# Optimization experiments

Measured on AMD Instinct MI355X. Metric: run time of the kernel, lower is better.

## Reference

```python
import jax, jax.numpy as jnp
import numpy as np

N_U, N_I, D, Q, NNZ, L = 100000, 100000, 64, 128, 3200000, 3
N = N_U + N_I

def setup_inputs() -> dict:
    key = jax.random.key(0)
    ks = jax.random.split(key, 9)
    user_emb = jax.random.normal(ks[0], (N_U, D), dtype=jnp.float32) * 0.1
    item_emb = jax.random.normal(ks[1], (N_I, D), dtype=jnp.float32) * 0.1
    adj_row = jax.random.randint(ks[2], (NNZ,), 0, N, dtype=jnp.int32)
    adj_col = jax.random.randint(ks[3], (NNZ,), 0, N, dtype=jnp.int32)
    # ~degree-normalized values so L-layer propagation stays stable
    adj_vals = jax.random.uniform(ks[4], (NNZ,), dtype=jnp.float32) / 16.0
    ut = jax.random.normal(ks[5], (Q, N_U), dtype=jnp.float32) * (1.0 / np.sqrt(N_U))
    vt = jax.random.normal(ks[6], (Q, N_I), dtype=jnp.float32) * (1.0 / np.sqrt(N_I))
    u_mul_s = jax.random.normal(ks[7], (N_U, Q), dtype=jnp.float32) * 0.1
    v_mul_s = jax.random.normal(ks[8], (N_I, Q), dtype=jnp.float32) * 0.1
    return {"user_emb": user_emb, "item_emb": item_emb, "adj_row": adj_row,
            "adj_col": adj_col, "adj_vals": adj_vals, "ut": ut, "vt": vt,
            "u_mul_s": u_mul_s, "v_mul_s": v_mul_s}

def _spmm(row, col, vals, x):
    # y[r] = sum_{e: row[e]==r} vals[e] * x[col[e]]
    return jax.ops.segment_sum(vals[:, None] * x[col], row, num_segments=N)

def reference(user_emb, item_emb, adj_row, adj_col, adj_vals, ut, vt, u_mul_s, v_mul_s):
    ego = jnp.concatenate([user_emb, item_emb], axis=0)  # [N, D]
    acc = jnp.zeros_like(ego)
    svd_u = jnp.zeros((N_U, D), dtype=ego.dtype)
    svd_i = jnp.zeros((N_I, D), dtype=ego.dtype)
    for _ in range(L):
        ego = _spmm(adj_row, adj_col, adj_vals, ego)
        acc = acc + ego
        ue, ie = ego[:N_U], ego[N_U:]
        ut_eu = ut @ ue            # [Q, D]
        vt_ei = vt @ ie            # [Q, D]
        svd_u = svd_u + u_mul_s @ vt_ei
        svd_i = svd_i + v_mul_s @ ut_eu
    mean = acc / L                 # mean over stacked layer embeddings
    return (mean[:N_U], svd_u, mean[N_U:], svd_i)
```

## Files before the change

kernel.cpp:

```cpp
#include <hip/hip_runtime.h>

constexpr int N_U  = 100000;
constexpr int N_I  = 100000;
constexpr int NTOT = 200000;
constexpr int D    = 64;
constexpr int Q    = 128;
constexpr int NNZ  = 3200000;
constexpr int SEG  = N_U * D;

constexpr int G1_CHUNK = 400;
constexpr int G1_NBLK  = 250;

constexpr int BROWS   = 512;
constexpr int NBUCK   = (NTOT + BROWS - 1) / BROWS;
constexpr int P_CHUNK = 8192;
constexpr int P_NBLK  = (NNZ + P_CHUNK - 1) / P_CHUNK;

constexpr int G2_R    = 64;
constexpr int G2_NBLK = (N_U + G2_R - 1) / G2_R;
constexpr int MSTRIDE = 132;

__device__ __forceinline__ unsigned short f2bf(float f) {
  unsigned int b = __float_as_uint(f);
  return (unsigned short)((b + 0x7fff + ((b >> 16) & 1)) >> 16);
}
__device__ __forceinline__ float bf2f(unsigned short u) {
  return __uint_as_float((unsigned int)u << 16);
}

__global__ void __launch_bounds__(512) k_bhist(const int* __restrict__ row,
                                               int* __restrict__ part) {
  __shared__ int h[NBUCK];
  const int t = threadIdx.x;
  if (t < NBUCK) h[t] = 0;
  __syncthreads();
  const int e0 = blockIdx.x * P_CHUNK;
#pragma unroll
  for (int i = 0; i < P_CHUNK / 512; ++i) {
    int e = e0 + i * 512 + t;
    if (e < NNZ) atomicAdd(&h[row[e] >> 9], 1);
  }
  __syncthreads();
  if (t < NBUCK) part[blockIdx.x * NBUCK + t] = h[t];
}

__global__ void __launch_bounds__(512) k_bscan(int* __restrict__ part,
                                               int* __restrict__ outb,
                                               int* __restrict__ bbase) {
  __shared__ int s[512];
  const int t = threadIdx.x;
  int run = 0;
  if (t < NBUCK) {
    for (int blk = 0; blk < P_NBLK; ++blk) {
      int v = part[blk * NBUCK + t];
      outb[blk * NBUCK + t] = run;
      run += v;
    }
  }
  const int own = (t < NBUCK) ? run : 0;
  s[t] = own;
  __syncthreads();
  for (int off = 1; off < 512; off <<= 1) {
    int y = (t >= off) ? s[t - off] : 0;
    __syncthreads();
    s[t] += y;
    __syncthreads();
  }
  int excl = s[t] - own;
  if (t <= NBUCK) bbase[t] = excl;
}

__global__ void __launch_bounds__(512) k_mscat(const int* __restrict__ row,
                                               const int* __restrict__ col,
                                               const float* __restrict__ val,
                                               const int* __restrict__ outb,
                                               const int* __restrict__ bbase,
                                               int2* __restrict__ ebuck) {
  __shared__ int cur[NBUCK];
  const int t = threadIdx.x;
  if (t < NBUCK) cur[t] = bbase[t] + outb[blockIdx.x * NBUCK + t];
  __syncthreads();
  const int e0 = blockIdx.x * P_CHUNK;
#pragma unroll
  for (int i = 0; i < P_CHUNK / 512; ++i) {
    int e = e0 + i * 512 + t;
    if (e < NNZ) {
      int r = row[e];
      int b = r >> 9;
      int pos = atomicAdd(&cur[b], 1);
      ebuck[pos] = make_int2(col[e] | ((r & (BROWS - 1)) << 18), __float_as_int(val[e]));
    }
  }
}

__global__ void __launch_bounds__(512) k_rsort(const int* __restrict__ bbase,
                                               const int2* __restrict__ ebuck,
                                               int2* __restrict__ edges,
                                               int* __restrict__ rowptr) {
  __shared__ int s[512];
  __shared__ int cur[512];
  const int t = threadIdx.x;
  const int b = blockIdx.x;
  const int eb0 = bbase[b], eb1 = bbase[b + 1];
  cur[t] = 0;
  __syncthreads();
  for (int e = eb0 + t; e < eb1; e += 512) atomicAdd(&cur[ebuck[e].x >> 18], 1);
  __syncthreads();
  const int own = cur[t];
  s[t] = own;
  __syncthreads();
  for (int off = 1; off < 512; off <<= 1) {
    int y = (t >= off) ? s[t - off] : 0;
    __syncthreads();
    s[t] += y;
    __syncthreads();
  }
  const int excl = s[t] - own;
  const int r = (b << 9) + t;
  if (r < NTOT) rowptr[r] = eb0 + excl;
  if (b == NBUCK - 1 && t == 0) rowptr[NTOT] = NNZ;
  cur[t] = eb0 + excl;
  __syncthreads();
  for (int e = eb0 + t; e < eb1; e += 512) {
    int2 kv = ebuck[e];
    int pos = atomicAdd(&cur[kv.x >> 18], 1);
    edges[pos] = make_int2(kv.x & 0x3FFFF, kv.y);
  }
}

__global__ void k_cvt(const float* __restrict__ user_emb,
                      const float* __restrict__ item_emb,
                      unsigned short* __restrict__ e0) {
  int i = blockIdx.x * 256 + threadIdx.x;
  if (i >= NTOT * D / 8) return;
  size_t base = (size_t)i * 8;
  const float* src = (base < (size_t)SEG) ? (user_emb + base) : (item_emb + base - SEG);
  float4 v0 = *reinterpret_cast<const float4*>(src);
  float4 v1 = *reinterpret_cast<const float4*>(src + 4);
  union { unsigned short us[8]; uint4 u4; } pk;
  pk.us[0] = f2bf(v0.x); pk.us[1] = f2bf(v0.y); pk.us[2] = f2bf(v0.z); pk.us[3] = f2bf(v0.w);
  pk.us[4] = f2bf(v1.x); pk.us[5] = f2bf(v1.y); pk.us[6] = f2bf(v1.z); pk.us[7] = f2bf(v1.w);
  *reinterpret_cast<uint4*>(e0 + base) = pk.u4;
}

__global__ void k_spmm(const int* __restrict__ rowptr, const int2* __restrict__ edges,
                       const unsigned short* __restrict__ src,
                       unsigned short* __restrict__ dst) {
  const int r = (blockIdx.x * 256 + threadIdx.x) >> 6;
  const int lane = threadIdx.x & 63;
  if (r >= NTOT) return;
  const int e0 = rowptr[r], e1 = rowptr[r + 1];
  float sum = 0.f;
  int e = e0;
  for (; e + 8 <= e1; e += 8) {
    int2 d0 = edges[e + 0], d1 = edges[e + 1], d2 = edges[e + 2], d3 = edges[e + 3];
    int2 d4 = edges[e + 4], d5 = edges[e + 5], d6 = edges[e + 6], d7 = edges[e + 7];
    unsigned short u0 = src[((size_t)d0.x << 6) + lane];
    unsigned short u1 = src[((size_t)d1.x << 6) + lane];
    unsigned short u2 = src[((size_t)d2.x << 6) + lane];
    unsigned short u3 = src[((size_t)d3.x << 6) + lane];
    unsigned short u4 = src[((size_t)d4.x << 6) + lane];
    unsigned short u5 = src[((size_t)d5.x << 6) + lane];
    unsigned short u6 = src[((size_t)d6.x << 6) + lane];
    unsigned short u7 = src[((size_t)d7.x << 6) + lane];
    sum = fmaf(__int_as_float(d0.y), bf2f(u0), sum);
    sum = fmaf(__int_as_float(d1.y), bf2f(u1), sum);
    sum = fmaf(__int_as_float(d2.y), bf2f(u2), sum);
    sum = fmaf(__int_as_float(d3.y), bf2f(u3), sum);
    sum = fmaf(__int_as_float(d4.y), bf2f(u4), sum);
    sum = fmaf(__int_as_float(d5.y), bf2f(u5), sum);
    sum = fmaf(__int_as_float(d6.y), bf2f(u6), sum);
    sum = fmaf(__int_as_float(d7.y), bf2f(u7), sum);
  }
  for (; e + 2 <= e1; e += 2) {
    int2 d0 = edges[e + 0], d1 = edges[e + 1];
    unsigned short u0 = src[((size_t)d0.x << 6) + lane];
    unsigned short u1 = src[((size_t)d1.x << 6) + lane];
    sum = fmaf(__int_as_float(d0.y), bf2f(u0), sum);
    sum = fmaf(__int_as_float(d1.y), bf2f(u1), sum);
  }
  if (e < e1) {
    int2 d0 = edges[e];
    sum = fmaf(__int_as_float(d0.y), bf2f(src[((size_t)d0.x << 6) + lane]), sum);
  }
  dst[((size_t)r << 6) + lane] = f2bf(sum);
}

__global__ void k_mean(const unsigned short* __restrict__ e1,
                       const unsigned short* __restrict__ e2,
                       const unsigned short* __restrict__ e3,
                       float* __restrict__ mean_u, float* __restrict__ mean_i) {
  int i = blockIdx.x * 256 + threadIdx.x;
  if (i >= NTOT * D / 8) return;
  size_t base = (size_t)i * 8;
  uint4 a = *reinterpret_cast<const uint4*>(e1 + base);
  uint4 b = *reinterpret_cast<const uint4*>(e2 + base);
  uint4 c = *reinterpret_cast<const uint4*>(e3 + base);
  union { uint4 u4; unsigned short us[8]; } ua, ub, uc;
  ua.u4 = a; ub.u4 = b; uc.u4 = c;
  float o[8];
#pragma unroll
  for (int j = 0; j < 8; ++j)
    o[j] = (bf2f(ua.us[j]) + bf2f(ub.us[j]) + bf2f(uc.us[j])) * (1.f / 3.f);
  float* dstp = (base < (size_t)SEG) ? (mean_u + base) : (mean_i + base - SEG);
  *reinterpret_cast<float4*>(dstp) = make_float4(o[0], o[1], o[2], o[3]);
  *reinterpret_cast<float4*>(dstp + 4) = make_float4(o[4], o[5], o[6], o[7]);
}

__global__ void __launch_bounds__(512) k_g1(const float* __restrict__ ut,
                                            const float* __restrict__ vt,
                                            const float* __restrict__ accu,
                                            const float* __restrict__ acci,
                                            float* __restrict__ Ppart) {
  __shared__ float Wl[128 * 65];
  __shared__ float Xl[64 * 64];
  const int mat = blockIdx.y;
  const float* __restrict__ W = mat ? vt : ut;
  const float* __restrict__ X = mat ? acci : accu;
  const int t = threadIdx.x;
  const int q0 = (t >> 4) * 4;
  const int d0 = (t & 15) * 4;
  const int n0 = blockIdx.x * G1_CHUNK;
  const int n1 = min(n0 + G1_CHUNK, N_U);
  float4 a0 = {0, 0, 0, 0}, a1 = {0, 0, 0, 0}, a2 = {0, 0, 0, 0}, a3 = {0, 0, 0, 0};
  for (int k = n0; k < n1; k += 64) {
#pragma unroll
    for (int rep = 0; rep < 2; ++rep) {
      int f4 = t + rep * 512;
      int row = f4 >> 4;
      int c4 = (f4 & 15) * 4;
      int gr = k + row;
      float4 v = (gr < n1) ? *reinterpret_cast<const float4*>(X + (size_t)gr * 64 + c4)
                           : float4{0, 0, 0, 0};
      *reinterpret_cast<float4*>(&Xl[row * 64 + c4]) = v;
    }
    {
      int q = t >> 2;
      int c16 = (t & 3) * 16;
#pragma unroll
      for (int jj = 0; jj < 4; ++jj) {
        int kk = c16 + jj * 4;
        int gk = k + kk;
        float4 v = (gk < n1) ? *reinterpret_cast<const float4*>(W + (size_t)q * N_U + gk)
                             : float4{0, 0, 0, 0};
        *reinterpret_cast<float4*>(&Wl[q * 65 + kk]) = v;
      }
    }
    __syncthreads();
#pragma unroll 2
    for (int kk = 0; kk < 64; kk += 4) {
      float4 w0 = *reinterpret_cast<const float4*>(&Wl[(q0 + 0) * 65 + kk]);
      float4 w1 = *reinterpret_cast<const float4*>(&Wl[(q0 + 1) * 65 + kk]);
      float4 w2 = *reinterpret_cast<const float4*>(&Wl[(q0 + 2) * 65 + kk]);
      float4 w3 = *reinterpret_cast<const float4*>(&Wl[(q0 + 3) * 65 + kk]);
      float4 x0 = *reinterpret_cast<const float4*>(&Xl[(kk + 0) * 64 + d0]);
      float4 x1 = *reinterpret_cast<const float4*>(&Xl[(kk + 1) * 64 + d0]);
      float4 x2 = *reinterpret_cast<const float4*>(&Xl[(kk + 2) * 64 + d0]);
      float4 x3 = *reinterpret_cast<const float4*>(&Xl[(kk + 3) * 64 + d0]);
#define FMA16(aj, wj)                                                                 \
  aj.x = fmaf(wj.x, x0.x, aj.x); aj.y = fmaf(wj.x, x0.y, aj.y);                       \
  aj.z = fmaf(wj.x, x0.z, aj.z); aj.w = fmaf(wj.x, x0.w, aj.w);                       \
  aj.x = fmaf(wj.y, x1.x, aj.x); aj.y = fmaf(wj.y, x1.y, aj.y);                       \
  aj.z = fmaf(wj.y, x1.z, aj.z); aj.w = fmaf(wj.y, x1.w, aj.w);                       \
  aj.x = fmaf(wj.z, x2.x, aj.x); aj.y = fmaf(wj.z, x2.y, aj.y);                       \
  aj.z = fmaf(wj.z, x2.z, aj.z); aj.w = fmaf(wj.z, x2.w, aj.w);                       \
  aj.x = fmaf(wj.w, x3.x, aj.x); aj.y = fmaf(wj.w, x3.y, aj.y);                       \
  aj.z = fmaf(wj.w, x3.z, aj.z); aj.w = fmaf(wj.w, x3.w, aj.w);
      FMA16(a0, w0)
      FMA16(a1, w1)
      FMA16(a2, w2)
      FMA16(a3, w3)
#undef FMA16
    }
    __syncthreads();
  }
  float* dst = Ppart + ((size_t)mat * G1_NBLK + blockIdx.x) * (Q * D);
  *reinterpret_cast<float4*>(dst + (q0 + 0) * 64 + d0) = a0;
  *reinterpret_cast<float4*>(dst + (q0 + 1) * 64 + d0) = a1;
  *reinterpret_cast<float4*>(dst + (q0 + 2) * 64 + d0) = a2;
  *reinterpret_cast<float4*>(dst + (q0 + 3) * 64 + d0) = a3;
}

__global__ void k_reduce(const float* __restrict__ Ppart, float* __restrict__ P) {
  int idx = blockIdx.x * 256 + threadIdx.x;
  if (idx >= 2 * Q * D) return;
  int mat = idx >> 13;
  int qd = idx & (Q * D - 1);
  const float* src = Ppart + (size_t)mat * G1_NBLK * (Q * D) + qd;
  float s = 0.f;
#pragma unroll 4
  for (int b = 0; b < G1_NBLK; ++b) s += src[(size_t)b * (Q * D)];
  P[idx] = s * 3.f;
}

__global__ void __launch_bounds__(256) k_g2(const float* __restrict__ u_mul_s,
                                            const float* __restrict__ v_mul_s,
                                            const float* __restrict__ P,
                                            float* __restrict__ svd_u,
                                            float* __restrict__ svd_i) {
  __shared__ float Pl[Q * D];
  __shared__ float Ml[G2_R * MSTRIDE];
  const int mat = blockIdx.y;
  const float* __restrict__ M  = mat ? v_mul_s : u_mul_s;
  const float* __restrict__ Pg = mat ? P : (P + Q * D);
  float* __restrict__ outp     = mat ? svd_i : svd_u;
  const int t = threadIdx.x;
  const int r0 = blockIdx.x * G2_R;
#pragma unroll
  for (int i = 0; i < 8; ++i) {
    int idx = i * 256 + t;
    reinterpret_cast<float4*>(Pl)[idx] = reinterpret_cast<const float4*>(Pg)[idx];
  }
#pragma unroll
  for (int pass = 0; pass < 8; ++pass) {
    int row = pass * 8 + (t >> 5);
    int c4 = (t & 31) * 4;
    int gr = r0 + row;
    float4 v = (gr < N_U) ? *reinterpret_cast<const float4*>(M + (size_t)gr * Q + c4)
                          : float4{0, 0, 0, 0};
    *reinterpret_cast<float4*>(&Ml[row * MSTRIDE + c4]) = v;
  }
  __syncthreads();
  const int rb = (t >> 4) * 4;
  const int c0 = (t & 15) * 4;
  float4 a0 = {0, 0, 0, 0}, a1 = {0, 0, 0, 0}, a2 = {0, 0, 0, 0}, a3 = {0, 0, 0, 0};
#pragma unroll 8
  for (int kk = 0; kk < Q; kk += 4) {
    float4 m0 = *reinterpret_cast<const float4*>(&Ml[(rb + 0) * MSTRIDE + kk]);
    float4 m1 = *reinterpret_cast<const float4*>(&Ml[(rb + 1) * MSTRIDE + kk]);
    float4 m2 = *reinterpret_cast<const float4*>(&Ml[(rb + 2) * MSTRIDE + kk]);
    float4 m3 = *reinterpret_cast<const float4*>(&Ml[(rb + 3) * MSTRIDE + kk]);
    float4 p0 = *reinterpret_cast<const float4*>(&Pl[(kk + 0) * D + c0]);
    float4 p1 = *reinterpret_cast<const float4*>(&Pl[(kk + 1) * D + c0]);
    float4 p2 = *reinterpret_cast<const float4*>(&Pl[(kk + 2) * D + c0]);
    float4 p3 = *reinterpret_cast<const float4*>(&Pl[(kk + 3) * D + c0]);
#define G2FMA(aj, mj)                                                                 \
  aj.x = fmaf(mj.x, p0.x, aj.x); aj.y = fmaf(mj.x, p0.y, aj.y);                       \
  aj.z = fmaf(mj.x, p0.z, aj.z); aj.w = fmaf(mj.x, p0.w, aj.w);                       \
  aj.x = fmaf(mj.y, p1.x, aj.x); aj.y = fmaf(mj.y, p1.y, aj.y);                       \
  aj.z = fmaf(mj.y, p1.z, aj.z); aj.w = fmaf(mj.y, p1.w, aj.w);                       \
  aj.x = fmaf(mj.z, p2.x, aj.x); aj.y = fmaf(mj.z, p2.y, aj.y);                       \
  aj.z = fmaf(mj.z, p2.z, aj.z); aj.w = fmaf(mj.z, p2.w, aj.w);                       \
  aj.x = fmaf(mj.w, p3.x, aj.x); aj.y = fmaf(mj.w, p3.y, aj.y);                       \
  aj.z = fmaf(mj.w, p3.z, aj.z); aj.w = fmaf(mj.w, p3.w, aj.w);
    G2FMA(a0, m0)
    G2FMA(a1, m1)
    G2FMA(a2, m2)
    G2FMA(a3, m3)
#undef G2FMA
  }
  const int gr = r0 + rb;
  if (gr + 0 < N_U) *reinterpret_cast<float4*>(outp + (size_t)(gr + 0) * D + c0) = a0;
  if (gr + 1 < N_U) *reinterpret_cast<float4*>(outp + (size_t)(gr + 1) * D + c0) = a1;
  if (gr + 2 < N_U) *reinterpret_cast<float4*>(outp + (size_t)(gr + 2) * D + c0) = a2;
  if (gr + 3 < N_U) *reinterpret_cast<float4*>(outp + (size_t)(gr + 3) * D + c0) = a3;
}

extern "C" void kernel_launch(void* const* d_in, const int* in_sizes, int n_in,
                              void* d_out, int out_size, void* d_ws, size_t ws_size,
                              hipStream_t stream) {
  const float* user_emb = (const float*)d_in[0];
  const float* item_emb = (const float*)d_in[1];
  const int*   adj_row  = (const int*)d_in[2];
  const int*   adj_col  = (const int*)d_in[3];
  const float* adj_vals = (const float*)d_in[4];
  const float* ut       = (const float*)d_in[5];
  const float* vt       = (const float*)d_in[6];
  const float* u_mul_s  = (const float*)d_in[7];
  const float* v_mul_s  = (const float*)d_in[8];
  float* out = (float*)d_out;

  char* ws = (char*)d_ws;
  size_t off = 0;
  auto alloc = [&](size_t bytes) -> void* {
    void* p = ws + off;
    off = (off + bytes + 255) & ~(size_t)255;
    return p;
  };
  unsigned short* eb0 = (unsigned short*)alloc((size_t)NTOT * D * 2);
  unsigned short* eb1 = (unsigned short*)alloc((size_t)NTOT * D * 2);
  unsigned short* eb2 = (unsigned short*)alloc((size_t)NTOT * D * 2);
  unsigned short* eb3 = (unsigned short*)alloc((size_t)NTOT * D * 2);
  int2*  ebuck  = (int2*)alloc((size_t)NNZ * 8);
  int2*  edges  = (int2*)alloc((size_t)NNZ * 8);
  int*   rowptr = (int*)alloc((size_t)(NTOT + 1) * 4);
  int*   part   = (int*)alloc((size_t)P_NBLK * NBUCK * 4);
  int*   outb   = (int*)alloc((size_t)P_NBLK * NBUCK * 4);
  int*   bbase  = (int*)alloc((size_t)(NBUCK + 1) * 4);
  float* P      = (float*)alloc(2 * Q * D * 4);
  float* Ppart  = (float*)alloc((size_t)2 * G1_NBLK * Q * D * 4);

  float* mean_u = out;
  float* svd_u  = out + (size_t)SEG;
  float* mean_i = out + 2 * (size_t)SEG;
  float* svd_i  = out + 3 * (size_t)SEG;

  k_bhist<<<P_NBLK, 512, 0, stream>>>(adj_row, part);
  k_bscan<<<1, 512, 0, stream>>>(part, outb, bbase);
  k_mscat<<<P_NBLK, 512, 0, stream>>>(adj_row, adj_col, adj_vals, outb, bbase, ebuck);
  k_rsort<<<NBUCK, 512, 0, stream>>>(bbase, ebuck, edges, rowptr);

  k_cvt<<<(NTOT * D / 8 + 255) / 256, 256, 0, stream>>>(user_emb, item_emb, eb0);

  const int spmmGrid = (NTOT * 64) / 256;
  k_spmm<<<spmmGrid, 256, 0, stream>>>(rowptr, edges, eb0, eb1);
  k_spmm<<<spmmGrid, 256, 0, stream>>>(rowptr, edges, eb1, eb2);
  k_spmm<<<spmmGrid, 256, 0, stream>>>(rowptr, edges, eb2, eb3);

  k_mean<<<(NTOT * D / 8 + 255) / 256, 256, 0, stream>>>(eb1, eb2, eb3, mean_u, mean_i);

  k_g1<<<dim3(G1_NBLK, 2), 512, 0, stream>>>(ut, vt, mean_u, mean_i, Ppart);
  k_reduce<<<(2 * Q * D + 255) / 256, 256, 0, stream>>>(Ppart, P);

  k_g2<<<dim3(G2_NBLK, 2), 256, 0, stream>>>(u_mul_s, v_mul_s, P, svd_u, svd_i);
}
```

Baseline: 703.3 us.

## Restructure k_g2 into K-tiled double-buffered GEMM with swizzled LDS and 8x4 register tile

The final dense projection kernel now processes 128 rows per block, loading M and P in 32-wide K tiles into double-buffered shared memory with an XOR swizzle instead of padding. Each thread accumulates an 8x4 output tile instead of 4x4, which raises FMA work per LDS load and cuts shared memory use so more blocks can be resident. The risks are more registers per thread and a sync on every K step, and the kernel is only a small part of the total runtime.

```diff
diff --git a/kernel.cpp b/kernel.cpp
--- a/kernel.cpp
+++ b/kernel.cpp
@@ -16,9 +16,9 @@
 constexpr int P_CHUNK = 8192;
 constexpr int P_NBLK  = (NNZ + P_CHUNK - 1) / P_CHUNK;
 
-constexpr int G2_R    = 64;
-constexpr int G2_NBLK = (N_U + G2_R - 1) / G2_R;
-constexpr int MSTRIDE = 132;
+constexpr int G2_ROWS = 128;
+constexpr int G2_KT   = 32;
+constexpr int G2_NBLK = (N_U + G2_ROWS - 1) / G2_ROWS;
 
 __device__ __forceinline__ unsigned short f2bf(float f) {
   unsigned int b = __float_as_uint(f);
@@ -298,62 +298,83 @@
                                             const float* __restrict__ P,
                                             float* __restrict__ svd_u,
                                             float* __restrict__ svd_i) {
-  __shared__ float Pl[Q * D];
-  __shared__ float Ml[G2_R * MSTRIDE];
+  __shared__ float4 Ml4[2][G2_ROWS][8];
+  __shared__ float  Pl[2][G2_KT][64];
   const int mat = blockIdx.y;
   const float* __restrict__ M  = mat ? v_mul_s : u_mul_s;
   const float* __restrict__ Pg = mat ? P : (P + Q * D);
   float* __restrict__ outp     = mat ? svd_i : svd_u;
   const int t = threadIdx.x;
-  const int r0 = blockIdx.x * G2_R;
-#pragma unroll
-  for (int i = 0; i < 8; ++i) {
-    int idx = i * 256 + t;
-    reinterpret_cast<float4*>(Pl)[idx] = reinterpret_cast<const float4*>(Pg)[idx];
-  }
-#pragma unroll
-  for (int pass = 0; pass < 8; ++pass) {
-    int row = pass * 8 + (t >> 5);
-    int c4 = (t & 31) * 4;
-    int gr = r0 + row;
-    float4 v = (gr < N_U) ? *reinterpret_cast<const float4*>(M + (size_t)gr * Q + c4)
-                          : float4{0, 0, 0, 0};
-    *reinterpret_cast<float4*>(&Ml[row * MSTRIDE + c4]) = v;
-  }
-  __syncthreads();
-  const int rb = (t >> 4) * 4;
-  const int c0 = (t & 15) * 4;
-  float4 a0 = {0, 0, 0, 0}, a1 = {0, 0, 0, 0}, a2 = {0, 0, 0, 0}, a3 = {0, 0, 0, 0};
-#pragma unroll 8
-  for (int kk = 0; kk < Q; kk += 4) {
-    float4 m0 = *reinterpret_cast<const float4*>(&Ml[(rb + 0) * MSTRIDE + kk]);
-    float4 m1 = *reinterpret_cast<const float4*>(&Ml[(rb + 1) * MSTRIDE + kk]);
-    float4 m2 = *reinterpret_cast<const float4*>(&Ml[(rb + 2) * MSTRIDE + kk]);
-    float4 m3 = *reinterpret_cast<const float4*>(&Ml[(rb + 3) * MSTRIDE + kk]);
-    float4 p0 = *reinterpret_cast<const float4*>(&Pl[(kk + 0) * D + c0]);
-    float4 p1 = *reinterpret_cast<const float4*>(&Pl[(kk + 1) * D + c0]);
-    float4 p2 = *reinterpret_cast<const float4*>(&Pl[(kk + 2) * D + c0]);
-    float4 p3 = *reinterpret_cast<const float4*>(&Pl[(kk + 3) * D + c0]);
-#define G2FMA(aj, mj)                                                                 \
-  aj.x = fmaf(mj.x, p0.x, aj.x); aj.y = fmaf(mj.x, p0.y, aj.y);                       \
-  aj.z = fmaf(mj.x, p0.z, aj.z); aj.w = fmaf(mj.x, p0.w, aj.w);                       \
-  aj.x = fmaf(mj.y, p1.x, aj.x); aj.y = fmaf(mj.y, p1.y, aj.y);                       \
-  aj.z = fmaf(mj.y, p1.z, aj.z); aj.w = fmaf(mj.y, p1.w, aj.w);                       \
-  aj.x = fmaf(mj.z, p2.x, aj.x); aj.y = fmaf(mj.z, p2.y, aj.y);                       \
-  aj.z = fmaf(mj.z, p2.z, aj.z); aj.w = fmaf(mj.z, p2.w, aj.w);                       \
-  aj.x = fmaf(mj.w, p3.x, aj.x); aj.y = fmaf(mj.w, p3.y, aj.y);                       \
-  aj.z = fmaf(mj.w, p3.z, aj.z); aj.w = fmaf(mj.w, p3.w, aj.w);
-    G2FMA(a0, m0)
-    G2FMA(a1, m1)
-    G2FMA(a2, m2)
-    G2FMA(a3, m3)
-#undef G2FMA
-  }
-  const int gr = r0 + rb;
-  if (gr + 0 < N_U) *reinterpret_cast<float4*>(outp + (size_t)(gr + 0) * D + c0) = a0;
-  if (gr + 1 < N_U) *reinterpret_cast<float4*>(outp + (size_t)(gr + 1) * D + c0) = a1;
-  if (gr + 2 < N_U) *reinterpret_cast<float4*>(outp + (size_t)(gr + 2) * D + c0) = a2;
-  if (gr + 3 < N_U) *reinterpret_cast<float4*>(outp + (size_t)(gr + 3) * D + c0) = a3;
+  const int r0 = blockIdx.x * G2_ROWS;
+
+  auto stage = [&](int kt, int buf) {
+#pragma unroll
+    for (int i = 0; i < 4; ++i) {
+      int f4 = i * 256 + t;
+      int row = f4 >> 3;
+      int kf4 = f4 & 7;
+      int gr = r0 + row;
+      float4 v = {0, 0, 0, 0};
+      if (gr < N_U)
+        v = *reinterpret_cast<const float4*>(M + (size_t)gr * Q + kt * G2_KT + kf4 * 4);
+      Ml4[buf][row][kf4 ^ ((row >> 3) & 7)] = v;
+    }
+#pragma unroll
+    for (int i = 0; i < 2; ++i) {
+      int f4 = i * 256 + t;
+      int k = f4 >> 4;
+      int c4 = (f4 & 15) * 4;
+      *reinterpret_cast<float4*>(&Pl[buf][k][c4]) =
+          *reinterpret_cast<const float4*>(Pg + (size_t)(kt * G2_KT + k) * 64 + c4);
+    }
+  };
+
+  const int cg = t & 15;
+  const int rg = t >> 4;
+  const int c0 = cg * 4;
+  const int rb = rg * 8;
+  const int swz = rg & 7;
+
+  float4 a[8];
+#pragma unroll
+  for (int rr = 0; rr < 8; ++rr) a[rr] = float4{0, 0, 0, 0};
+
+  stage(0, 0);
+  __syncthreads();
+#pragma unroll
+  for (int kt = 0; kt < 4; ++kt) {
+    const int buf = kt & 1;
+    if (kt < 3) stage(kt + 1, buf ^ 1);
+#pragma unroll
+    for (int kk = 0; kk < G2_KT; kk += 4) {
+      float4 p0 = *reinterpret_cast<const float4*>(&Pl[buf][kk + 0][c0]);
+      float4 p1 = *reinterpret_cast<const float4*>(&Pl[buf][kk + 1][c0]);
+      float4 p2 = *reinterpret_cast<const float4*>(&Pl[buf][kk + 2][c0]);
+      float4 p3 = *reinterpret_cast<const float4*>(&Pl[buf][kk + 3][c0]);
+      const int ks = (kk >> 2) ^ swz;
+#define G2ROW(rr)                                                                     \
+  {                                                                                   \
+    float4 m = Ml4[buf][rb + rr][ks];                                                 \
+    a[rr].x = fmaf(m.x, p0.x, a[rr].x); a[rr].y = fmaf(m.x, p0.y, a[rr].y);           \
+    a[rr].z = fmaf(m.x, p0.z, a[rr].z); a[rr].w = fmaf(m.x, p0.w, a[rr].w);           \
+    a[rr].x = fmaf(m.y, p1.x, a[rr].x); a[rr].y = fmaf(m.y, p1.y, a[rr].y);           \
+    a[rr].z = fmaf(m.y, p1.z, a[rr].z); a[rr].w = fmaf(m.y, p1.w, a[rr].w);           \
+    a[rr].x = fmaf(m.z, p2.x, a[rr].x); a[rr].y = fmaf(m.z, p2.y, a[rr].y);           \
+    a[rr].z = fmaf(m.z, p2.z, a[rr].z); a[rr].w = fmaf(m.z, p2.w, a[rr].w);           \
+    a[rr].x = fmaf(m.w, p3.x, a[rr].x); a[rr].y = fmaf(m.w, p3.y, a[rr].y);           \
+    a[rr].z = fmaf(m.w, p3.z, a[rr].z); a[rr].w = fmaf(m.w, p3.w, a[rr].w);           \
+  }
+      G2ROW(0) G2ROW(1) G2ROW(2) G2ROW(3) G2ROW(4) G2ROW(5) G2ROW(6) G2ROW(7)
+#undef G2ROW
+    }
+    __syncthreads();
+  }
+#pragma unroll
+  for (int rr = 0; rr < 8; ++rr) {
+    int gr = r0 + rb + rr;
+    if (gr < N_U)
+      *reinterpret_cast<float4*>(outp + (size_t)gr * D + c0) = a[rr];
+  }
 }
 
 extern "C" void kernel_launch(void* const* d_in, const int* in_sizes, int n_in,
```

After: 2.299 ms. 227% more time.
